# Performance work log

Measured on AMD Instinct MI355X. Metric: run time of the kernel, lower is better.

## Reference

```python
import jax, jax.numpy as jnp
import numpy as np
import math

H = 128      # hidden_size
B = 4        # bsz
N = 32       # bsz * num_doc_per_q
L = 128      # doc_len


def setup_inputs() -> dict:
    key = jax.random.key(0)
    ks = jax.random.split(key, 7)
    word_ent_info = jax.random.normal(ks[0], (N, L, H), dtype=jnp.float32)
    word_ent_info_mask = jax.random.randint(ks[1], (N, L), 0, 2, dtype=jnp.int32)
    doc = jax.random.normal(ks[2], (N, L, H), dtype=jnp.float32)
    doc_mask = jax.random.randint(ks[3], (N, L), 0, 2, dtype=jnp.int32)
    q_for_text = jax.random.normal(ks[4], (B, H), dtype=jnp.float32)
    # nn.Linear(3H, H): weight [H, 3H], bias [H]
    W1 = jax.random.normal(ks[5], (H, 3 * H), dtype=jnp.float32) / math.sqrt(3 * H)
    b1 = jnp.zeros((H,), dtype=jnp.float32)
    # nn.Linear(H, 1): weight [1, H], bias [1]
    w2 = jax.random.normal(ks[6], (1, H), dtype=jnp.float32) / math.sqrt(H)
    b2 = jnp.zeros((1,), dtype=jnp.float32)
    return {"word_ent_info": word_ent_info, "word_ent_info_mask": word_ent_info_mask,
            "doc": doc, "doc_mask": doc_mask, "q_for_text": q_for_text,
            "W1": W1, "b1": b1, "w2": w2, "b2": b2}


def reference(word_ent_info, word_ent_info_mask, doc, doc_mask, q_for_text, W1, b1, w2, b2):
    n, l, h = doc.shape
    bsz = q_for_text.shape[0]
    dt = doc.dtype

    # word_ent_infoagg = mask^T @ word_ent_info -> [N, H]
    m = word_ent_info_mask.astype(dt)
    ent_agg = jnp.einsum('nl,nlh->nh', m, word_ent_info)

    # q expanded to one row per document: [N, H]
    q_exp = jnp.repeat(q_for_text, n // bsz, axis=0)

    # Split W1 over the concat([doc_self, ent_agg, q_agg]) feature axis.
    # score_pre[n,j,k,:] = W1a @ (doc_j*doc_k) + W1b @ (doc_j*ent_agg) + W1c @ (doc_k*q)
    W1a, W1b, W1c = jnp.split(W1, 3, axis=1)        # each [H, H]
    A = jnp.einsum('nje,nke,ge->njkg', doc, doc, W1a)          # [N,L,L,H]
    Bt = jnp.einsum('nje,ge->njg', doc * ent_agg[:, None, :], W1b)  # [N,L,H]
    Ct = jnp.einsum('nke,ge->nkg', doc * q_exp[:, None, :], W1c)    # [N,L,H]
    hid = jnp.tanh(A + Bt[:, :, None, :] + Ct[:, None, :, :] + b1)  # [N,L,L,H]

    score = (jnp.einsum('njkg,g->njk', hid, w2[0]) + b2[0]) / math.sqrt(h)

    dm = doc_mask.astype(dt)
    score_mask = dm[:, :, None] * dm[:, None, :]     # [N,L,L]
    score = jnp.where(score_mask == 0.0, jnp.asarray(-1e9, dt), score)
    w = jax.nn.softmax(score, axis=-1) * score_mask
    doc_ent_enc = jnp.einsum('njk,nkh->njh', w, doc)  # [N,L,H]
    return doc_ent_enc
```

## Files before the change

### kernel.cpp

```cpp
#include <hip/hip_runtime.h>
#include <hip/hip_bf16.h>
#include <math.h>

#define Hh 128
#define Nn 32
#define Ll 128
#define W1S 384
#define PAD 136

typedef __attribute__((ext_vector_type(8))) short short8;
typedef __attribute__((ext_vector_type(4))) float floatx4;

__device__ __forceinline__ unsigned short f2bf(float x) {
  __hip_bfloat16 h = __float2bfloat16(x);
  return __builtin_bit_cast(unsigned short, h);
}

__device__ __forceinline__ short8 pack8(float4 a, float4 b) {
  short8 r;
  r[0] = (short)f2bf(a.x); r[1] = (short)f2bf(a.y);
  r[2] = (short)f2bf(a.z); r[3] = (short)f2bf(a.w);
  r[4] = (short)f2bf(b.x); r[5] = (short)f2bf(b.y);
  r[6] = (short)f2bf(b.z); r[7] = (short)f2bf(b.w);
  return r;
}

__global__ void k_entagg(const float* __restrict__ wei, const int* __restrict__ wmask,
                         float* __restrict__ ent) {
  __shared__ float red[2][Hh];
  int n = blockIdx.x, tid = threadIdx.x;
  int e = tid & 127, half = tid >> 7;
  const float* wp = wei + (size_t)n * Ll * Hh + (size_t)half * 64 * Hh + e;
  const int* mp = wmask + n * Ll + half * 64;
  float a = 0.f;
#pragma unroll 8
  for (int l = 0; l < 64; ++l)
    a = fmaf((float)mp[l], wp[(size_t)l * Hh], a);
  red[half][e] = a;
  __syncthreads();
  if (tid < Hh) ent[n * Hh + tid] = red[0][tid] + red[1][tid];
}

__launch_bounds__(256, 2)
__global__ void k_btct(const float* __restrict__ doc, const float* __restrict__ q,
                       const float* __restrict__ W1, const float* __restrict__ ent,
                       float* __restrict__ Bt, float* __restrict__ Ct) {
  __shared__ __align__(16) short Xs[Hh * PAD];
  __shared__ __align__(16) short Ws[Hh * PAD];
  __shared__ __align__(16) float ms[Hh];
  int bid = blockIdx.x;
  int n = bid >> 1, which = bid & 1;
  int tid = threadIdx.x;
  const float* docn = doc + (size_t)n * Ll * Hh;
  const float* mv = which ? (q + (n >> 3) * Hh) : (ent + n * Hh);
  if (tid < Hh) ms[tid] = mv[tid];
  __syncthreads();
  const float* wbase = W1 + Hh + which * Hh;
#pragma unroll
  for (int p = 0; p < 8; ++p) {
    int idx = p * 256 + tid;
    int row = idx >> 4;
    int e8 = (idx & 15) * 8;
    const float4* wp = (const float4*)(wbase + (size_t)row * W1S + e8);
    float4 w0 = wp[0], w1 = wp[1];
    *(short8*)(Ws + row * PAD + e8) = pack8(w0, w1);
    const float4* dp = (const float4*)(docn + (size_t)row * Hh + e8);
    float4 d0 = dp[0], d1 = dp[1];
    const float4* mp4 = (const float4*)(ms + e8);
    float4 m0 = mp4[0], m1 = mp4[1];
    d0.x *= m0.x; d0.y *= m0.y; d0.z *= m0.z; d0.w *= m0.w;
    d1.x *= m1.x; d1.y *= m1.y; d1.z *= m1.z; d1.w *= m1.w;
    *(short8*)(Xs + row * PAD + e8) = pack8(d0, d1);
  }
  __syncthreads();

  int lane = tid & 63, w = tid >> 6;
  int l15 = lane & 15, quad = lane >> 4;
  floatx4 acc[2][8];
#pragma unroll
  for (int mt = 0; mt < 2; ++mt)
#pragma unroll
    for (int nt = 0; nt < 8; ++nt)
      acc[mt][nt] = (floatx4){0.f, 0.f, 0.f, 0.f};
#pragma unroll
  for (int e0 = 0; e0 < Hh; e0 += 32) {
    int eo = e0 + quad * 8;
    short8 af[2], bfr[8];
    af[0] = *(const short8*)(Xs + (w * 32 + l15) * PAD + eo);
    af[1] = *(const short8*)(Xs + (w * 32 + 16 + l15) * PAD + eo);
#pragma unroll
    for (int nt = 0; nt < 8; ++nt)
      bfr[nt] = *(const short8*)(Ws + (nt * 16 + l15) * PAD + eo);
#pragma unroll
    for (int mt = 0; mt < 2; ++mt)
#pragma unroll
      for (int nt = 0; nt < 8; ++nt)
        acc[mt][nt] = __builtin_amdgcn_mfma_f32_16x16x32_bf16(af[mt], bfr[nt], acc[mt][nt], 0, 0, 0);
  }
  float* outp = (which ? Ct : Bt) + (size_t)n * Ll * Hh;
#pragma unroll
  for (int mt = 0; mt < 2; ++mt)
#pragma unroll
    for (int nt = 0; nt < 8; ++nt)
#pragma unroll
      for (int r = 0; r < 4; ++r) {
        int k = w * 32 + mt * 16 + quad * 4 + r;
        outp[(size_t)k * Hh + nt * 16 + l15] = acc[mt][nt][r];
      }
}

__launch_bounds__(256, 2)
__global__ void k_main(const float* __restrict__ doc, const int* __restrict__ dmask,
                       const float* __restrict__ W1, const float* __restrict__ b1,
                       const float* __restrict__ w2, const float* __restrict__ b2,
                       const float* __restrict__ Bt, const float* __restrict__ Ct,
                       float* __restrict__ out) {
  __shared__ __align__(16) short As[Hh * PAD];
  __shared__ __align__(16) short Bs[Hh * PAD];
  __shared__ __align__(16) float djs[Hh];
  __shared__ __align__(16) float sc[Ll];
  __shared__ float rbuf[8];

  int bid = blockIdx.x;
  int n = bid >> 7, j = bid & 127;
  int tid = threadIdx.x;
  const float* docn = doc + (size_t)n * Ll * Hh;
  size_t orow = ((size_t)n * Ll + j) * Hh;

  if (dmask[n * Ll + j] == 0) {
    if (tid < Hh) out[orow + tid] = 0.f;
    return;
  }

  if (tid < Hh) djs[tid] = docn[(size_t)j * Hh + tid];
  __syncthreads();

#pragma unroll
  for (int p = 0; p < 8; ++p) {
    int idx = p * 256 + tid;
    int row = idx >> 4;
    int e8 = (idx & 15) * 8;
    const float4* wp = (const float4*)(W1 + (size_t)row * W1S + e8);
    float4 w0 = wp[0], w1 = wp[1];
    *(short8*)(As + row * PAD + e8) = pack8(w0, w1);
    const float4* dp = (const float4*)(docn + (size_t)row * Hh + e8);
    float4 d0 = dp[0], d1 = dp[1];
    const float4* jp = (const float4*)(djs + e8);
    float4 j0 = jp[0], j1 = jp[1];
    d0.x *= j0.x; d0.y *= j0.y; d0.z *= j0.z; d0.w *= j0.w;
    d1.x *= j1.x; d1.y *= j1.y; d1.z *= j1.z; d1.w *= j1.w;
    *(short8*)(Bs + row * PAD + e8) = pack8(d0, d1);
  }
  __syncthreads();

  int lane = tid & 63, w = tid >> 6;
  int l15 = lane & 15, quad = lane >> 4;
  floatx4 acc[2][8];
#pragma unroll
  for (int mt = 0; mt < 2; ++mt)
#pragma unroll
    for (int nt = 0; nt < 8; ++nt)
      acc[mt][nt] = (floatx4){0.f, 0.f, 0.f, 0.f};
#pragma unroll
  for (int e0 = 0; e0 < Hh; e0 += 32) {
    int eo = e0 + quad * 8;
    short8 af[2], bfr[8];
    af[0] = *(const short8*)(Bs + (w * 32 + l15) * PAD + eo);
    af[1] = *(const short8*)(Bs + (w * 32 + 16 + l15) * PAD + eo);
#pragma unroll
    for (int nt = 0; nt < 8; ++nt)
      bfr[nt] = *(const short8*)(As + (nt * 16 + l15) * PAD + eo);
#pragma unroll
    for (int mt = 0; mt < 2; ++mt)
#pragma unroll
      for (int nt = 0; nt < 8; ++nt)
        acc[mt][nt] = __builtin_amdgcn_mfma_f32_16x16x32_bf16(af[mt], bfr[nt], acc[mt][nt], 0, 0, 0);
  }

  const float c2 = 2.885390081777927f;
  float bbc[8], w2r[8];
  const float* btrow = Bt + orow;
#pragma unroll
  for (int nt = 0; nt < 8; ++nt) {
    int g = nt * 16 + l15;
    bbc[nt] = (btrow[g] + b1[g]) * c2;
    w2r[nt] = w2[g];
  }
  const float* ctn = Ct + (size_t)n * Ll * Hh;
#pragma unroll
  for (int mt = 0; mt < 2; ++mt) {
#pragma unroll
    for (int r = 0; r < 4; ++r) {
      int k = w * 32 + mt * 16 + quad * 4 + r;
      const float* ctp = ctn + (size_t)k * Hh + l15;
      float p = 0.f;
#pragma unroll
      for (int nt = 0; nt < 8; ++nt) {
        float s = acc[mt][nt][r] + ctp[nt * 16];
        float a2 = fmaf(s, c2, bbc[nt]);
        float e = exp2f(a2);
        float th = fmaf(-2.f, __builtin_amdgcn_rcpf(e + 1.f), 1.f);
        p = fmaf(th, w2r[nt], p);
      }
      p += __shfl_xor(p, 1);
      p += __shfl_xor(p, 2);
      p += __shfl_xor(p, 4);
      p += __shfl_xor(p, 8);
      if (l15 == 0) sc[k] = p;
    }
  }
  __syncthreads();

  float b2v = b2[0];
  const float inv = 0.088388347648318447f;
  if (tid < Ll) {
    float s = (sc[tid] + b2v) * inv;
    sc[tid] = dmask[n * Ll + tid] ? s : -1e9f;
  }
  __syncthreads();
  if (tid < Ll) {
    float m = sc[tid];
#pragma unroll
    for (int off = 32; off; off >>= 1) m = fmaxf(m, __shfl_xor(m, off));
    if ((tid & 63) == 0) rbuf[tid >> 6] = m;
  }
  __syncthreads();
  float mx = fmaxf(rbuf[0], rbuf[1]);
  if (tid < Ll) {
    float e = __expf(sc[tid] - mx);
    sc[tid] = e;
    float ssum = e;
#pragma unroll
    for (int off = 32; off; off >>= 1) ssum += __shfl_xor(ssum, off);
    if ((tid & 63) == 0) rbuf[4 + (tid >> 6)] = ssum;
  }
  __syncthreads();
  float rden = 1.f / (rbuf[4] + rbuf[5]);
  if (tid < Ll)
    sc[tid] = dmask[n * Ll + tid] ? sc[tid] * rden : 0.f;
  __syncthreads();

  float* ored = (float*)As;
  int half = tid >> 7, h = tid & 127;
  const float* dbase = docn + (size_t)half * 64 * Hh + h;
  float o = 0.f;
#pragma unroll 8
  for (int kk = 0; kk < 64; ++kk)
    o = fmaf(sc[half * 64 + kk], dbase[(size_t)kk * Hh], o);
  ored[half * Hh + h] = o;
  __syncthreads();
  if (tid < Ll) out[orow + tid] = ored[tid] + ored[Hh + tid];
}

extern "C" void kernel_launch(void* const* d_in, const int* in_sizes, int n_in,
                              void* d_out, int out_size, void* d_ws, size_t ws_size,
                              hipStream_t stream) {
  const float* wei   = (const float*)d_in[0];
  const int*   wmask = (const int*)d_in[1];
  const float* doc   = (const float*)d_in[2];
  const int*   dmask = (const int*)d_in[3];
  const float* q     = (const float*)d_in[4];
  const float* W1    = (const float*)d_in[5];
  const float* b1    = (const float*)d_in[6];
  const float* w2    = (const float*)d_in[7];
  const float* b2    = (const float*)d_in[8];
  float* out = (float*)d_out;

  float* ws  = (float*)d_ws;
  float* ent = ws;
  float* Bt  = ws + Nn * Hh;
  float* Ct  = Bt + (size_t)Nn * Ll * Hh;

  k_entagg<<<Nn, 256, 0, stream>>>(wei, wmask, ent);
  k_btct<<<2 * Nn, 256, 0, stream>>>(doc, q, W1, ent, Bt, Ct);
  k_main<<<Nn * Ll, 256, 0, stream>>>(doc, dmask, W1, b1, w2, b2, Bt, Ct, out);
}
```

Before: 136.6 us.

## Fuse entity aggregation with Bt/Ct projection and streamline main-kernel softmax

Merges the entity-aggregation kernel and the Bt/Ct projection kernel into one prep kernel per document. It stages the doc tile once in bf16 and scales it by ent or q in registers before the MFMAs, which removes one launch and the ent round-trip through global memory. The prep grid halves to 32 blocks, each computing both products serially, so parallelism drops. In the main kernel the block index is remapped so adjacent blocks take different documents. The doc row j is read straight into registers instead of through shared memory, and the softmax now runs in a single wavefront with fewer barriers.

```diff
diff --git a/kernel.cpp b/kernel.cpp
--- a/kernel.cpp
+++ b/kernel.cpp
@@ -15,7 +15,10 @@
   __hip_bfloat16 h = __float2bfloat16(x);
   return __builtin_bit_cast(unsigned short, h);
 }
-
+__device__ __forceinline__ float bf2f(short s) {
+  unsigned int u = ((unsigned int)(unsigned short)s) << 16;
+  return __builtin_bit_cast(float, u);
+}
 __device__ __forceinline__ short8 pack8(float4 a, float4 b) {
   short8 r;
   r[0] = (short)f2bf(a.x); r[1] = (short)f2bf(a.y);
@@ -25,88 +28,107 @@
   return r;
 }
 
-__global__ void k_entagg(const float* __restrict__ wei, const int* __restrict__ wmask,
-                         float* __restrict__ ent) {
-  __shared__ float red[2][Hh];
+__launch_bounds__(256, 1)
+__global__ void k_prep(const float* __restrict__ wei, const int* __restrict__ wmask,
+                       const float* __restrict__ doc, const float* __restrict__ q,
+                       const float* __restrict__ W1,
+                       float* __restrict__ Bt, float* __restrict__ Ct) {
+  __shared__ __align__(16) short docb[Hh * PAD];
+  __shared__ __align__(16) short Wb[Hh * PAD];
+  __shared__ __align__(16) short Wc[Hh * PAD];
+  __shared__ __align__(16) float entL[Hh];
+  __shared__ __align__(16) float qL[Hh];
+  __shared__ __align__(16) float red[2][Hh];
+
   int n = blockIdx.x, tid = threadIdx.x;
-  int e = tid & 127, half = tid >> 7;
-  const float* wp = wei + (size_t)n * Ll * Hh + (size_t)half * 64 * Hh + e;
-  const int* mp = wmask + n * Ll + half * 64;
-  float a = 0.f;
+  const float* docn = doc + (size_t)n * Ll * Hh;
+  int e8 = (tid & 15) * 8;
+
+#pragma unroll
+  for (int p = 0; p < 8; ++p) {
+    int row = p * 16 + (tid >> 4);
+    const float4* dp = (const float4*)(docn + (size_t)row * Hh + e8);
+    *(short8*)(docb + row * PAD + e8) = pack8(dp[0], dp[1]);
+    const float4* wbp = (const float4*)(W1 + (size_t)row * W1S + Hh + e8);
+    *(short8*)(Wb + row * PAD + e8) = pack8(wbp[0], wbp[1]);
+    const float4* wcp = (const float4*)(W1 + (size_t)row * W1S + 2 * Hh + e8);
+    *(short8*)(Wc + row * PAD + e8) = pack8(wcp[0], wcp[1]);
+  }
+  {
+    int e = tid & 127, half = tid >> 7;
+    const float* wp = wei + (size_t)n * Ll * Hh + (size_t)half * 64 * Hh + e;
+    const int* mp = wmask + n * Ll + half * 64;
+    float a = 0.f;
 #pragma unroll 8
-  for (int l = 0; l < 64; ++l)
-    a = fmaf((float)mp[l], wp[(size_t)l * Hh], a);
-  red[half][e] = a;
-  __syncthreads();
-  if (tid < Hh) ent[n * Hh + tid] = red[0][tid] + red[1][tid];
-}
-
-__launch_bounds__(256, 2)
-__global__ void k_btct(const float* __restrict__ doc, const float* __restrict__ q,
-                       const float* __restrict__ W1, const float* __restrict__ ent,
-                       float* __restrict__ Bt, float* __restrict__ Ct) {
-  __shared__ __align__(16) short Xs[Hh * PAD];
-  __shared__ __align__(16) short Ws[Hh * PAD];
-  __shared__ __align__(16) float ms[Hh];
-  int bid = blockIdx.x;
-  int n = bid >> 1, which = bid & 1;
-  int tid = threadIdx.x;
-  const float* docn = doc + (size_t)n * Ll * Hh;
-  const float* mv = which ? (q + (n >> 3) * Hh) : (ent + n * Hh);
-  if (tid < Hh) ms[tid] = mv[tid];
-  __syncthreads();
-  const float* wbase = W1 + Hh + which * Hh;
-#pragma unroll
-  for (int p = 0; p < 8; ++p) {
-    int idx = p * 256 + tid;
-    int row = idx >> 4;
-    int e8 = (idx & 15) * 8;
-    const float4* wp = (const float4*)(wbase + (size_t)row * W1S + e8);
-    float4 w0 = wp[0], w1 = wp[1];
-    *(short8*)(Ws + row * PAD + e8) = pack8(w0, w1);
-    const float4* dp = (const float4*)(docn + (size_t)row * Hh + e8);
-    float4 d0 = dp[0], d1 = dp[1];
-    const float4* mp4 = (const float4*)(ms + e8);
-    float4 m0 = mp4[0], m1 = mp4[1];
-    d0.x *= m0.x; d0.y *= m0.y; d0.z *= m0.z; d0.w *= m0.w;
-    d1.x *= m1.x; d1.y *= m1.y; d1.z *= m1.z; d1.w *= m1.w;
-    *(short8*)(Xs + row * PAD + e8) = pack8(d0, d1);
-  }
+    for (int l = 0; l < 64; ++l) a = fmaf((float)mp[l], wp[(size_t)l * Hh], a);
+    red[half][e] = a;
+  }
+  if (tid < Hh) qL[tid] = q[(n >> 3) * Hh + tid];
+  __syncthreads();
+  if (tid < Hh) entL[tid] = red[0][tid] + red[1][tid];
   __syncthreads();
 
   int lane = tid & 63, w = tid >> 6;
   int l15 = lane & 15, quad = lane >> 4;
-  floatx4 acc[2][8];
+
+  float ef[32], qf[32];
+#pragma unroll
+  for (int c = 0; c < 4; ++c)
+#pragma unroll
+    for (int i = 0; i < 8; ++i) {
+      int e = c * 32 + quad * 8 + i;
+      ef[c * 8 + i] = entL[e];
+      qf[c * 8 + i] = qL[e];
+    }
+  short8 draw[2][4];
 #pragma unroll
   for (int mt = 0; mt < 2; ++mt)
 #pragma unroll
-    for (int nt = 0; nt < 8; ++nt)
-      acc[mt][nt] = (floatx4){0.f, 0.f, 0.f, 0.f};
-#pragma unroll
-  for (int e0 = 0; e0 < Hh; e0 += 32) {
-    int eo = e0 + quad * 8;
-    short8 af[2], bfr[8];
-    af[0] = *(const short8*)(Xs + (w * 32 + l15) * PAD + eo);
-    af[1] = *(const short8*)(Xs + (w * 32 + 16 + l15) * PAD + eo);
-#pragma unroll
-    for (int nt = 0; nt < 8; ++nt)
-      bfr[nt] = *(const short8*)(Ws + (nt * 16 + l15) * PAD + eo);
+    for (int c = 0; c < 4; ++c)
+      draw[mt][c] = *(const short8*)(docb + (w * 32 + mt * 16 + l15) * PAD + c * 32 + quad * 8);
+
+  for (int which = 0; which < 2; ++which) {
+    const short* Ws = which ? Wc : Wb;
+    const float* sf = which ? qf : ef;
+    floatx4 acc[2][8];
 #pragma unroll
     for (int mt = 0; mt < 2; ++mt)
 #pragma unroll
+      for (int nt = 0; nt < 8; ++nt) acc[mt][nt] = (floatx4){0.f, 0.f, 0.f, 0.f};
+#pragma unroll
+    for (int c = 0; c < 4; ++c) {
+      short8 af[2];
+#pragma unroll
+      for (int mt = 0; mt < 2; ++mt) {
+        float t[8];
+#pragma unroll
+        for (int i = 0; i < 8; ++i) t[i] = bf2f(draw[mt][c][i]) * sf[c * 8 + i];
+        short8 r;
+#pragma unroll
+        for (int i = 0; i < 8; ++i) r[i] = (short)f2bf(t[i]);
+        af[mt] = r;
+      }
+      short8 bfr[8];
+#pragma unroll
       for (int nt = 0; nt < 8; ++nt)
-        acc[mt][nt] = __builtin_amdgcn_mfma_f32_16x16x32_bf16(af[mt], bfr[nt], acc[mt][nt], 0, 0, 0);
-  }
-  float* outp = (which ? Ct : Bt) + (size_t)n * Ll * Hh;
-#pragma unroll
-  for (int mt = 0; mt < 2; ++mt)
-#pragma unroll
-    for (int nt = 0; nt < 8; ++nt)
-#pragma unroll
-      for (int r = 0; r < 4; ++r) {
-        int k = w * 32 + mt * 16 + quad * 4 + r;
-        outp[(size_t)k * Hh + nt * 16 + l15] = acc[mt][nt][r];
-      }
+        bfr[nt] = *(const short8*)(Ws + (nt * 16 + l15) * PAD + c * 32 + quad * 8);
+#pragma unroll
+      for (int mt = 0; mt < 2; ++mt)
+#pragma unroll
+        for (int nt = 0; nt < 8; ++nt)
+          acc[mt][nt] = __builtin_amdgcn_mfma_f32_16x16x32_bf16(af[mt], bfr[nt], acc[mt][nt], 0, 0, 0);
+    }
+    float* outp = (which ? Ct : Bt) + (size_t)n * Ll * Hh;
+#pragma unroll
+    for (int mt = 0; mt < 2; ++mt)
+#pragma unroll
+      for (int nt = 0; nt < 8; ++nt)
+#pragma unroll
+        for (int r = 0; r < 4; ++r) {
+          int k = w * 32 + mt * 16 + quad * 4 + r;
+          outp[(size_t)k * Hh + nt * 16 + l15] = acc[mt][nt][r];
+        }
+  }
 }
 
 __launch_bounds__(256, 2)
@@ -117,12 +139,11 @@
                        float* __restrict__ out) {
   __shared__ __align__(16) short As[Hh * PAD];
   __shared__ __align__(16) short Bs[Hh * PAD];
-  __shared__ __align__(16) float djs[Hh];
   __shared__ __align__(16) float sc[Ll];
-  __shared__ float rbuf[8];
+  __shared__ __align__(16) float scw[Ll];
 
   int bid = blockIdx.x;
-  int n = bid >> 7, j = bid & 127;
+  int n = bid & 31, j = bid >> 5;
   int tid = threadIdx.x;
   const float* docn = doc + (size_t)n * Ll * Hh;
   size_t orow = ((size_t)n * Ll + j) * Hh;
@@ -132,21 +153,16 @@
     return;
   }
 
-  if (tid < Hh) djs[tid] = docn[(size_t)j * Hh + tid];
-  __syncthreads();
-
+  int e8 = (tid & 15) * 8;
+  const float4* jp = (const float4*)(docn + (size_t)j * Hh + e8);
+  float4 j0 = jp[0], j1 = jp[1];
 #pragma unroll
   for (int p = 0; p < 8; ++p) {
-    int idx = p * 256 + tid;
-    int row = idx >> 4;
-    int e8 = (idx & 15) * 8;
+    int row = p * 16 + (tid >> 4);
     const float4* wp = (const float4*)(W1 + (size_t)row * W1S + e8);
-    float4 w0 = wp[0], w1 = wp[1];
-    *(short8*)(As + row * PAD + e8) = pack8(w0, w1);
+    *(short8*)(As + row * PAD + e8) = pack8(wp[0], wp[1]);
     const float4* dp = (const float4*)(docn + (size_t)row * Hh + e8);
     float4 d0 = dp[0], d1 = dp[1];
-    const float4* jp = (const float4*)(djs + e8);
-    float4 j0 = jp[0], j1 = jp[1];
     d0.x *= j0.x; d0.y *= j0.y; d0.z *= j0.z; d0.w *= j0.w;
     d1.x *= j1.x; d1.y *= j1.y; d1.z *= j1.z; d1.w *= j1.w;
     *(short8*)(Bs + row * PAD + e8) = pack8(d0, d1);
@@ -159,8 +175,7 @@
 #pragma unroll
   for (int mt = 0; mt < 2; ++mt)
 #pragma unroll
-    for (int nt = 0; nt < 8; ++nt)
-      acc[mt][nt] = (floatx4){0.f, 0.f, 0.f, 0.f};
+    for (int nt = 0; nt < 8; ++nt) acc[mt][nt] = (floatx4){0.f, 0.f, 0.f, 0.f};
 #pragma unroll
   for (int e0 = 0; e0 < Hh; e0 += 32) {
     int eo = e0 + quad * 8;
@@ -211,33 +226,26 @@
   }
   __syncthreads();
 
-  float b2v = b2[0];
-  const float inv = 0.088388347648318447f;
-  if (tid < Ll) {
-    float s = (sc[tid] + b2v) * inv;
-    sc[tid] = dmask[n * Ll + tid] ? s : -1e9f;
-  }
-  __syncthreads();
-  if (tid < Ll) {
-    float m = sc[tid];
-#pragma unroll
-    for (int off = 32; off; off >>= 1) m = fmaxf(m, __shfl_xor(m, off));
-    if ((tid & 63) == 0) rbuf[tid >> 6] = m;
-  }
-  __syncthreads();
-  float mx = fmaxf(rbuf[0], rbuf[1]);
-  if (tid < Ll) {
-    float e = __expf(sc[tid] - mx);
-    sc[tid] = e;
-    float ssum = e;
-#pragma unroll
-    for (int off = 32; off; off >>= 1) ssum += __shfl_xor(ssum, off);
-    if ((tid & 63) == 0) rbuf[4 + (tid >> 6)] = ssum;
-  }
-  __syncthreads();
-  float rden = 1.f / (rbuf[4] + rbuf[5]);
-  if (tid < Ll)
-    sc[tid] = dmask[n * Ll + tid] ? sc[tid] * rden : 0.f;
+  {
+    float b2v = b2[0];
+    const float inv = 0.088388347648318447f;
+    const int* dmn = dmask + n * Ll;
+    int m0 = dmn[lane], m1 = dmn[lane + 64];
+    float s0 = (sc[lane] + b2v) * inv;
+    float s1 = (sc[lane + 64] + b2v) * inv;
+    s0 = m0 ? s0 : -1e9f;
+    s1 = m1 ? s1 : -1e9f;
+    float mx = fmaxf(s0, s1);
+#pragma unroll
+    for (int off = 32; off; off >>= 1) mx = fmaxf(mx, __shfl_xor(mx, off));
+    float ex0 = __expf(s0 - mx), ex1 = __expf(s1 - mx);
+    float sm = ex0 + ex1;
+#pragma unroll
+    for (int off = 32; off; off >>= 1) sm += __shfl_xor(sm, off);
+    float rden = 1.f / sm;
+    scw[lane] = m0 ? ex0 * rden : 0.f;
+    scw[lane + 64] = m1 ? ex1 * rden : 0.f;
+  }
   __syncthreads();
 
   float* ored = (float*)As;
@@ -246,7 +254,7 @@
   float o = 0.f;
 #pragma unroll 8
   for (int kk = 0; kk < 64; ++kk)
-    o = fmaf(sc[half * 64 + kk], dbase[(size_t)kk * Hh], o);
+    o = fmaf(scw[half * 64 + kk], dbase[(size_t)kk * Hh], o);
   ored[half * Hh + h] = o;
   __syncthreads();
   if (tid < Ll) out[orow + tid] = ored[tid] + ored[Hh + tid];
@@ -266,12 +274,10 @@
   const float* b2    = (const float*)d_in[8];
   float* out = (float*)d_out;
 
-  float* ws  = (float*)d_ws;
-  float* ent = ws;
-  float* Bt  = ws + Nn * Hh;
-  float* Ct  = Bt + (size_t)Nn * Ll * Hh;
-
-  k_entagg<<<Nn, 256, 0, stream>>>(wei, wmask, ent);
-  k_btct<<<2 * Nn, 256, 0, stream>>>(doc, q, W1, ent, Bt, Ct);
+  float* ws = (float*)d_ws;
+  float* Bt = ws;
+  float* Ct = Bt + (size_t)Nn * Ll * Hh;
+
+  k_prep<<<Nn, 256, 0, stream>>>(wei, wmask, doc, q, W1, Bt, Ct);
   k_main<<<Nn * Ll, 256, 0, stream>>>(doc, dmask, W1, b1, w2, b2, Bt, Ct, out);
 }
```

New measurement: 136.3 us. About the same (-0.2%).
